# Kernel tuning notes

Measured on AMD Instinct MI355X. Metric: run time of the kernel, lower is better.

The kernel has to match this reference:

```python
import jax, jax.numpy as jnp
import numpy as np

N_NODES = 10000
N_EDGES = 320000
NODE_C = 256
IN_EDGE_C = 256
OUT_EDGE_C = 512
BN_EPS = 1e-5


def setup_inputs() -> dict:
    key = jax.random.key(0)
    ks = jax.random.split(key, 10)
    d_in = 2 * NODE_C + IN_EDGE_C  # 768
    x = jax.random.normal(ks[0], (N_NODES, NODE_C), dtype=jnp.float32)
    edge_index = jax.random.randint(ks[1], (2, N_EDGES), 0, N_NODES, dtype=jnp.int64)
    edge_attr = jax.random.normal(ks[2], (N_EDGES, IN_EDGE_C), dtype=jnp.float32)
    # MLP params (Linear stored as [in, out] for x @ W + b)
    W1 = jax.random.normal(ks[3], (d_in, OUT_EDGE_C), dtype=jnp.float32) / np.sqrt(d_in)
    b1 = jnp.zeros((OUT_EDGE_C,), dtype=jnp.float32)
    W2 = jax.random.normal(ks[4], (OUT_EDGE_C, OUT_EDGE_C), dtype=jnp.float32) / np.sqrt(OUT_EDGE_C)
    b2 = jnp.zeros((OUT_EDGE_C,), dtype=jnp.float32)
    # BatchNorm affine params
    gamma = jnp.ones((OUT_EDGE_C,), dtype=jnp.float32)
    beta = jnp.zeros((OUT_EDGE_C,), dtype=jnp.float32)
    return {"x": x, "edge_index": edge_index, "edge_attr": edge_attr,
            "W1": W1, "b1": b1, "W2": W2, "b2": b2,
            "gamma": gamma, "beta": beta}


def reference(x, edge_index, edge_attr, W1, b1, W2, b2, gamma, beta):
    src = edge_index[0]  # x_j (source / neighbor)
    dst = edge_index[1]  # x_i (target, aggregation index)
    x_i = x[dst]                                  # [E, node_c]
    x_j = x[src]                                  # [E, node_c]
    m = jnp.concatenate([x_i, x_j - x_i, edge_attr], axis=-1)  # [E, 2*node_c+edge_c]
    h = jax.nn.relu(m @ W1 + b1) @ W2 + b2        # per-edge MLP -> [E, out_c]
    out = jax.ops.segment_sum(h, dst, num_segments=x.shape[0])  # scatter-add -> [N, out_c]
    # BatchNorm1d (training-mode batch statistics, biased variance)
    mean = jnp.mean(out, axis=0)
    var = jnp.var(out, axis=0)
    y = (out - mean) * jax.lax.rsqrt(var + BN_EPS) * gamma + beta
    return jax.nn.relu(y)
```

## Files before the change

### kernel.cpp

```cpp
#include <hip/hip_runtime.h>
#include <hip/hip_bf16.h>
#include <cstdint>

#define NN 10000
#define NE 320000
#define NC 256
#define OC 512
#define K1 256

typedef __bf16 bf16_t;
typedef bf16_t bf16x8 __attribute__((ext_vector_type(8)));
typedef bf16_t bf16x4 __attribute__((ext_vector_type(4)));
typedef float  f32x4  __attribute__((ext_vector_type(4)));

__device__ __forceinline__ void gload_lds16(const void* g, void* l) {
  __builtin_amdgcn_global_load_lds(
      (const __attribute__((address_space(1))) unsigned int*)g,
      (__attribute__((address_space(3))) unsigned int*)l, 16, 0, 0);
}

__device__ __forceinline__ int permB(int R) {
  return (R & ~63) + ((R & 15) << 2) + ((R >> 4) & 3);
}

__global__ void k_prep(const float* __restrict__ x,
                       const float* __restrict__ W1,
                       const float* __restrict__ W2,
                       bf16_t* __restrict__ xb,
                       bf16_t* __restrict__ w1abt,
                       bf16_t* __restrict__ w1ct,
                       bf16_t* __restrict__ w2t,
                       float* __restrict__ agg,
                       int* __restrict__ deg,
                       int* __restrict__ cursor,
                       float* __restrict__ sums) {
  const int stride = gridDim.x * blockDim.x;
  for (int i = blockIdx.x * blockDim.x + threadIdx.x; i < NN * OC; i += stride) {
    agg[i] = 0.0f;
    if (i < NN * NC) xb[i] = (bf16_t)x[i];
    if (i < 1024 * K1) {
      const int n = i >> 8, k = i & 255;
      float w;
      if (n < OC) w = W1[(size_t)k * OC + n] - W1[(size_t)(k + NC) * OC + n];
      else        w = W1[(size_t)(k + NC) * OC + (n - OC)];
      w1abt[i] = (bf16_t)w;
    }
    if (i < OC * K1) {
      const int n = i >> 8, k = i & 255;
      w1ct[i] = (bf16_t)W1[(size_t)(512 + k) * OC + n];
    }
    if (i < OC * OC) {
      const int n = i >> 9, k = i & 511;
      w2t[i] = (bf16_t)W2[(size_t)k * OC + n];
    }
    if (i < NN) { deg[i] = 0; cursor[i] = 0; }
    if (i < 1024) sums[i] = 0.0f;
  }
}

__global__ void k_deg(const int* __restrict__ dstIdx, int* __restrict__ deg) {
  const int i = blockIdx.x * blockDim.x + threadIdx.x;
  if (i < NE) atomicAdd(&deg[dstIdx[i]], 1);
}

__global__ void k_scan(const int* __restrict__ deg, int* __restrict__ offs) {
  __shared__ int carry;
  __shared__ int wsum[4];
  if (threadIdx.x == 0) carry = 0;
  __syncthreads();
  const int lane = threadIdx.x & 63, w = threadIdx.x >> 6;
  for (int base = 0; base < NN; base += 256) {
    const int i = base + threadIdx.x;
    const int v = (i < NN) ? deg[i] : 0;
    int s = v;
#pragma unroll
    for (int d = 1; d < 64; d <<= 1) { int t = __shfl_up(s, d); if (lane >= d) s += t; }
    if (lane == 63) wsum[w] = s;
    __syncthreads();
    int woff = 0;
    for (int j = 0; j < w; j++) woff += wsum[j];
    const int incl = s + woff + carry;
    if (i < NN) offs[i] = incl - v;
    __syncthreads();
    if (threadIdx.x == 255) carry = incl;
    __syncthreads();
  }
}

__global__ void k_scatter(const int* __restrict__ srcIdx, const int* __restrict__ dstIdx,
                          const int* __restrict__ offs, int* __restrict__ cursor,
                          int* __restrict__ eperm, int* __restrict__ sdst,
                          int* __restrict__ ssrc) {
  const int e = blockIdx.x * blockDim.x + threadIdx.x;
  if (e < NE) {
    const int d = dstIdx[e];
    const int pos = offs[d] + atomicAdd(&cursor[d], 1);
    eperm[pos] = e;
    sdst[pos] = d;
    ssrc[pos] = srcIdx[e];
  }
}

__global__ __launch_bounds__(256) void k_pq(
    const bf16_t* __restrict__ xb,
    const bf16_t* __restrict__ w1abt,
    const float*  __restrict__ b1,
    float*        __restrict__ P,
    bf16_t*       __restrict__ Qb) {
  __shared__ bf16_t sA[128 * 64];
  __shared__ bf16_t sB[128 * 64];

  const int tid = threadIdx.x;
  const int cb = blockIdx.x & 7, rblk = blockIdx.x >> 3;
  const int r0 = rblk * 128, n0 = cb * 128;
  const int lane = tid & 63, wid = tid >> 6;
  const int mbase = (wid >> 1) * 64, nbase = (wid & 1) * 64;
  const int lr = lane >> 3, ls = lane & 7, slog = ls ^ lr;
  const int g = lane >> 4;

  f32x4 acc[4][4];
#pragma unroll
  for (int mi = 0; mi < 4; mi++)
#pragma unroll
    for (int ni = 0; ni < 4; ni++) acc[mi][ni] = (f32x4){0.f, 0.f, 0.f, 0.f};

  for (int kb = 0; kb < K1; kb += 64) {
#pragma unroll
    for (int i = 0; i < 4; i++) {
      const int row = wid * 32 + i * 8;
      int grow = r0 + row + lr;
      if (grow > NN - 1) grow = NN - 1;
      gload_lds16(xb + (size_t)grow * NC + kb + slog * 8, &sA[row * 64]);
      gload_lds16(w1abt + (size_t)(n0 + permB(row + lr)) * K1 + kb + slog * 8,
                  &sB[row * 64]);
    }
    __syncthreads();
#pragma unroll
    for (int kk = 0; kk < 2; kk++) {
      const int sl = kk * 4 + g;
      bf16x8 av[4], bv[4];
#pragma unroll
      for (int mi = 0; mi < 4; mi++) {
        const int rA = mbase + mi * 16 + (lane & 15);
        av[mi] = *(const bf16x8*)&sA[rA * 64 + ((sl ^ (rA & 7)) * 8)];
      }
#pragma unroll
      for (int ni = 0; ni < 4; ni++) {
        const int rB = nbase + ni * 16 + (lane & 15);
        bv[ni] = *(const bf16x8*)&sB[rB * 64 + ((sl ^ (rB & 7)) * 8)];
      }
#pragma unroll
      for (int mi = 0; mi < 4; mi++)
#pragma unroll
        for (int ni = 0; ni < 4; ni++)
          acc[mi][ni] = __builtin_amdgcn_mfma_f32_16x16x32_bf16(av[mi], bv[ni], acc[mi][ni], 0, 0, 0);
    }
    __syncthreads();
  }

  const int col0 = n0 + nbase + (lane & 15) * 4;
  f32x4 b1v = {0.f, 0.f, 0.f, 0.f};
  if (col0 < OC) b1v = *(const f32x4*)&b1[col0];
#pragma unroll
  for (int mi = 0; mi < 4; mi++) {
#pragma unroll
    for (int q = 0; q < 4; q++) {
      const int grow = r0 + mbase + mi * 16 + g * 4 + q;
      if (grow < NN) {
        if (col0 < OC) {
          f32x4 v;
#pragma unroll
          for (int j = 0; j < 4; j++) v[j] = acc[mi][j][q] + b1v[j];
          *(f32x4*)&P[(size_t)grow * OC + col0] = v;
        } else {
          bf16x4 v;
#pragma unroll
          for (int j = 0; j < 4; j++) v[j] = (bf16_t)acc[mi][j][q];
          *(bf16x4*)&Qb[(size_t)grow * OC + (col0 - OC)] = v;
        }
      }
    }
  }
}

__global__ __launch_bounds__(256, 2) void k_edge_gemm(
    const float*  __restrict__ ea,
    const bf16_t* __restrict__ w1ct,
    const float*  __restrict__ P,
    const bf16_t* __restrict__ Qb,
    const int*    __restrict__ eperm,
    const int*    __restrict__ sdst,
    const int*    __restrict__ ssrc,
    float*        __restrict__ agg) {
  __shared__ bf16_t sM[2][128 * 64];
  __shared__ bf16_t sW[2][128 * 64];
  __shared__ int sDst[128];
  __shared__ int sSrc[128];
  __shared__ int sE[128];

  const int bid0 = blockIdx.x;
  const int bid = (bid0 & 7) * 1250 + (bid0 >> 3);
  const int cb = bid & 3, eblk = bid >> 2;
  const int e0 = eblk * 128, n0 = cb * 128;

  const int tid = threadIdx.x;
  if (tid < 128) {
    sDst[tid] = sdst[e0 + tid];
    sSrc[tid] = ssrc[e0 + tid];
    sE[tid]   = eperm[e0 + tid];
  }
  __syncthreads();

  const int lane = tid & 63, wid = tid >> 6;
  const int mbase = (wid >> 1) * 64, nbase = (wid & 1) * 64;
  const int g = lane >> 4, r = lane & 15;
  const int lr = lane >> 3, ls = lane & 7, slogW = ls ^ lr;
  const int mrow = tid >> 1, qd = tid & 1;
  const int msw = mrow & 7;
  const float* eaRow = ea + (size_t)sE[mrow] * NC;

#define STAGE_W(kt, b)                                                        \
  _Pragma("unroll") for (int i = 0; i < 4; i++) {                             \
    const int rowb = wid * 32 + i * 8;                                        \
    gload_lds16(w1ct + (size_t)(n0 + permB(rowb + lr)) * K1 + (kt)*64 + slogW * 8, \
                &sW[b][rowb * 64]);                                           \
  }
#define LOAD_A(kt)                                                            \
  _Pragma("unroll") for (int j = 0; j < 8; j++)                               \
      a[j] = *(const f32x4*)(eaRow + (kt)*64 + qd * 32 + j * 4);
#define WRITE_M(b)                                                            \
  _Pragma("unroll") for (int tt = 0; tt < 4; tt++) {                          \
    const int slot = qd * 4 + tt;                                             \
    bf16x8 v;                                                                 \
    _Pragma("unroll") for (int jj = 0; jj < 4; jj++) {                        \
      v[jj] = (bf16_t)a[tt * 2][jj];                                          \
      v[4 + jj] = (bf16_t)a[tt * 2 + 1][jj];                                  \
    }                                                                         \
    *(bf16x8*)&sM[b][mrow * 64 + ((slot ^ msw) * 8)] = v;                     \
  }

  f32x4 a[8];

  STAGE_W(0, 0);
  LOAD_A(0);

  const int col0 = n0 + nbase + r * 4;
  f32x4  Pp[4][4];
  bf16x4 Qp[4][4];
#pragma unroll
  for (int mi = 0; mi < 4; mi++) {
    const int rbase = mbase + mi * 16 + g * 4;
#pragma unroll
    for (int q = 0; q < 4; q++) {
      Pp[mi][q] = *(const f32x4*)&P[(size_t)sDst[rbase + q] * OC + col0];
      Qp[mi][q] = *(const bf16x4*)&Qb[(size_t)sSrc[rbase + q] * OC + col0];
    }
  }

  WRITE_M(0);

  f32x4 acc[4][4];
#pragma unroll
  for (int mi = 0; mi < 4; mi++)
#pragma unroll
    for (int ni = 0; ni < 4; ni++) acc[mi][ni] = (f32x4){0.f, 0.f, 0.f, 0.f};

#pragma unroll
  for (int t = 0; t < 4; t++) {
    const int b = t & 1;
    __syncthreads();
    if (t < 3) { STAGE_W(t + 1, b ^ 1); LOAD_A(t + 1); }
#pragma unroll
    for (int kk = 0; kk < 2; kk++) {
      const int sl = kk * 4 + g;
      bf16x8 av[4], bv[4];
#pragma unroll
      for (int mi = 0; mi < 4; mi++) {
        const int rA = mbase + mi * 16 + r;
        av[mi] = *(const bf16x8*)&sM[b][rA * 64 + ((sl ^ (rA & 7)) * 8)];
      }
#pragma unroll
      for (int ni = 0; ni < 4; ni++) {
        const int rB = nbase + ni * 16 + r;
        bv[ni] = *(const bf16x8*)&sW[b][rB * 64 + ((sl ^ (rB & 7)) * 8)];
      }
#pragma unroll
      for (int mi = 0; mi < 4; mi++)
#pragma unroll
        for (int ni = 0; ni < 4; ni++)
          acc[mi][ni] = __builtin_amdgcn_mfma_f32_16x16x32_bf16(av[mi], bv[ni], acc[mi][ni], 0, 0, 0);
    }
    if (t < 3) { WRITE_M(b ^ 1); }
  }
#undef STAGE_W
#undef LOAD_A
#undef WRITE_M

#pragma unroll
  for (int mi = 0; mi < 4; mi++) {
    const int rbase = mbase + mi * 16 + g * 4;
    const int d0 = sDst[rbase],     d1 = sDst[rbase + 1];
    const int d2 = sDst[rbase + 2], d3 = sDst[rbase + 3];
    const int headId = d0, tailId = d3;
    const bool b1q = (d1 != d0), b2q = (d2 != d1), b3q = (d3 != d2);
    const bool seen = b1q | b2q | b3q;
    bool match[3];
#pragma unroll
    for (int j = 0; j < 3; j++) {
      const int tIdj = __shfl(tailId, (lane & 15) | (j << 4));
      match[j] = (j < g) && (tIdj == headId);
    }
    const int nextHead = __shfl(headId, (lane + 16) & 63);
    const bool endsHere = (g == 3) || (nextHead != tailId);

    f32x4 v0, v1, v2, v3;
#pragma unroll
    for (int j = 0; j < 4; j++) {
      v0[j] = fmaxf(acc[mi][j][0] + Pp[mi][0][j] + (float)Qp[mi][0][j], 0.f);
      v1[j] = fmaxf(acc[mi][j][1] + Pp[mi][1][j] + (float)Qp[mi][1][j], 0.f);
      v2[j] = fmaxf(acc[mi][j][2] + Pp[mi][2][j] + (float)Qp[mi][2][j], 0.f);
      v3[j] = fmaxf(acc[mi][j][3] + Pp[mi][3][j] + (float)Qp[mi][3][j], 0.f);
    }

    f32x4 head = {0.f, 0.f, 0.f, 0.f}, run = v0;
    bool first = true;
    if (b1q) { head = run; first = false; run = v1; } else run += v1;
    if (b2q) {
      if (first) { head = run; first = false; }
      else {
        float* base = agg + (size_t)d1 * OC + col0;
#pragma unroll
        for (int j = 0; j < 4; j++) if (run[j] != 0.f) atomicAdd(base + j, run[j]);
      }
      run = v2;
    } else run += v2;
    if (b3q) {
      if (first) { head = run; first = false; }
      else {
        float* base = agg + (size_t)d2 * OC + col0;
#pragma unroll
        for (int j = 0; j < 4; j++) if (run[j] != 0.f) atomicAdd(base + j, run[j]);
      }
      run = v3;
    } else run += v3;
    const f32x4 tailSum = run;

    f32x4 inc = {0.f, 0.f, 0.f, 0.f};
#pragma unroll
    for (int jg = 0; jg < 3; jg++) {
      f32x4 ts;
#pragma unroll
      for (int c = 0; c < 4; c++) ts[c] = __shfl(tailSum[c], (lane & 15) | (jg << 4));
      if (match[jg]) inc += ts;
    }
    if (seen) {
      float* base = agg + (size_t)headId * OC + col0;
#pragma unroll
      for (int j = 0; j < 4; j++) {
        const float h = head[j] + inc[j];
        if (h != 0.f) atomicAdd(base + j, h);
      }
    }
    if (endsHere) {
      float* base = agg + (size_t)tailId * OC + col0;
#pragma unroll
      for (int j = 0; j < 4; j++) {
        const float t = tailSum[j] + (seen ? 0.f : inc[j]);
        if (t != 0.f) atomicAdd(base + j, t);
      }
    }
  }
}

__global__ __launch_bounds__(256) void k_node_gemm(
    const float*  __restrict__ agg,
    const bf16_t* __restrict__ w2t,
    const float*  __restrict__ b2,
    const int*    __restrict__ deg,
    float*        __restrict__ out) {
  __shared__ bf16_t sM[128 * 72];
  __shared__ bf16_t sW[128 * 72];

  const int tid  = threadIdx.x;
  const int bid  = blockIdx.x;
  const int cb   = bid & 3;
  const int rblk = bid >> 2;
  const int r0   = rblk * 128;
  const int n0   = cb * 128;

  const int lane  = tid & 63, wid = tid >> 6;
  const int mbase = (wid >> 1) * 64, nbase = (wid & 1) * 64;
  const int se = tid >> 1;
  const int sk = (tid & 1) * 32;
  const int arow  = r0 + se;
  const bool rowok = arow < NN;

  f32x4 acc[4][4];
#pragma unroll
  for (int mi = 0; mi < 4; mi++)
#pragma unroll
    for (int ni = 0; ni < 4; ni++) acc[mi][ni] = (f32x4){0.f, 0.f, 0.f, 0.f};

  for (int kb = 0; kb < OC; kb += 64) {
    {
      bf16x8* dst = (bf16x8*)&sM[se * 72 + sk];
      if (rowok) {
        const float* pf = agg + (size_t)arow * OC + kb + sk;
        f32x4 f[8];
#pragma unroll
        for (int i = 0; i < 8; i++) f[i] = *(const f32x4*)(pf + i * 4);
#pragma unroll
        for (int i = 0; i < 4; i++) {
          bf16x8 v;
#pragma unroll
          for (int j = 0; j < 4; j++) {
            v[j]     = (bf16_t)f[2 * i][j];
            v[4 + j] = (bf16_t)f[2 * i + 1][j];
          }
          dst[i] = v;
        }
      } else {
        bf16x8 z = {};
        dst[0] = z; dst[1] = z; dst[2] = z; dst[3] = z;
      }
    }
    {
      const bf16_t* pw = w2t + (size_t)(n0 + permB(se)) * OC + kb + sk;
      bf16x8* dst = (bf16x8*)&sW[se * 72 + sk];
      dst[0] = *(const bf16x8*)(pw);
      dst[1] = *(const bf16x8*)(pw + 8);
      dst[2] = *(const bf16x8*)(pw + 16);
      dst[3] = *(const bf16x8*)(pw + 24);
    }
    __syncthreads();
#pragma unroll
    for (int kk = 0; kk < 2; kk++) {
      const int krd = kk * 32 + (lane >> 4) * 8;
      bf16x8 av[4], bv[4];
#pragma unroll
      for (int mi = 0; mi < 4; mi++)
        av[mi] = *(const bf16x8*)&sM[(mbase + mi * 16 + (lane & 15)) * 72 + krd];
#pragma unroll
      for (int ni = 0; ni < 4; ni++)
        bv[ni] = *(const bf16x8*)&sW[(nbase + ni * 16 + (lane & 15)) * 72 + krd];
#pragma unroll
      for (int mi = 0; mi < 4; mi++)
#pragma unroll
        for (int ni = 0; ni < 4; ni++)
          acc[mi][ni] = __builtin_amdgcn_mfma_f32_16x16x32_bf16(av[mi], bv[ni], acc[mi][ni], 0, 0, 0);
    }
    __syncthreads();
  }

  const int col0 = n0 + nbase + (lane & 15) * 4;
  const f32x4 b2v = *(const f32x4*)&b2[col0];
  const int g = lane >> 4;
#pragma unroll
  for (int mi = 0; mi < 4; mi++) {
#pragma unroll
    for (int q = 0; q < 4; q++) {
      const int row = r0 + mbase + mi * 16 + g * 4 + q;
      if (row < NN) {
        const float dg = (float)deg[row];
        f32x4 v;
#pragma unroll
        for (int j = 0; j < 4; j++) v[j] = acc[mi][j][q] + b2v[j] * dg;
        *(f32x4*)&out[(size_t)row * OC + col0] = v;
      }
    }
  }
}

__global__ void k_bn_stats(const float* __restrict__ out, float* __restrict__ sums) {
  const int c = threadIdx.x;
  float s1 = 0.f, q1 = 0.f, s2 = 0.f, q2 = 0.f;
  for (int n = blockIdx.x; n < NN; n += gridDim.x) {
    const float* row = out + (size_t)n * OC;
    const float v1 = row[c], v2 = row[c + 256];
    s1 += v1; q1 += v1 * v1;
    s2 += v2; q2 += v2 * v2;
  }
  atomicAdd(&sums[c], s1);        atomicAdd(&sums[OC + c], q1);
  atomicAdd(&sums[c + 256], s2);  atomicAdd(&sums[OC + c + 256], q2);
}

__global__ void k_bn_finalize(const float* __restrict__ sums,
                              const float* __restrict__ gamma,
                              const float* __restrict__ beta,
                              float* __restrict__ scale,
                              float* __restrict__ shift) {
  const int c = threadIdx.x;
  const float mean = sums[c] * (1.0f / NN);
  const float var  = sums[OC + c] * (1.0f / NN) - mean * mean;
  const float r    = rsqrtf(var + 1e-5f);
  const float sc   = r * gamma[c];
  scale[c] = sc;
  shift[c] = beta[c] - mean * sc;
}

__global__ void k_bn_apply(float* __restrict__ out,
                           const float* __restrict__ scale,
                           const float* __restrict__ shift) {
  const int i = blockIdx.x * blockDim.x + threadIdx.x;
  f32x4 v = *((const f32x4*)out + i);
  const int c = (i & 127) << 2;
  f32x4 r;
#pragma unroll
  for (int j = 0; j < 4; j++) r[j] = fmaxf(v[j] * scale[c + j] + shift[c + j], 0.0f);
  *((f32x4*)out + i) = r;
}

extern "C" void kernel_launch(void* const* d_in, const int* in_sizes, int n_in,
                              void* d_out, int out_size, void* d_ws, size_t ws_size,
                              hipStream_t stream) {
  const float* x     = (const float*)d_in[0];
  const int*   ei    = (const int*)d_in[1];
  const float* ea    = (const float*)d_in[2];
  const float* W1    = (const float*)d_in[3];
  const float* b1    = (const float*)d_in[4];
  const float* W2    = (const float*)d_in[5];
  const float* b2    = (const float*)d_in[6];
  const float* gamma = (const float*)d_in[7];
  const float* beta  = (const float*)d_in[8];
  float* out = (float*)d_out;

  char* ws = (char*)d_ws;
  float*  agg    = (float*)(ws);
  float*  P      = (float*)(ws + 20480000);
  bf16_t* Qb     = (bf16_t*)(ws + 40960000);
  bf16_t* xb     = (bf16_t*)(ws + 51200000);
  bf16_t* w1abt  = (bf16_t*)(ws + 56320000);
  bf16_t* w1ct   = (bf16_t*)(ws + 56844288);
  bf16_t* w2t    = (bf16_t*)(ws + 57106432);
  int*    deg    = (int*)(ws + 57630720);
  int*    offs   = (int*)(ws + 57670720);
  int*    cursor = (int*)(ws + 57710720);
  float*  sums   = (float*)(ws + 57750720);
  float*  scale  = (float*)(ws + 57754816);
  float*  shift  = (float*)(ws + 57756864);
  int*    eperm  = (int*)(ws + 57758912);
  int*    sdst   = (int*)(ws + 59038912);
  int*    ssrc   = (int*)(ws + 60318912);

  const int* srcIdx = ei;
  const int* dstIdx = ei + NE;

  k_prep<<<4096, 256, 0, stream>>>(x, W1, W2, xb, w1abt, w1ct, w2t, agg, deg, cursor, sums);
  k_deg<<<(NE + 255) / 256, 256, 0, stream>>>(dstIdx, deg);
  k_scan<<<1, 256, 0, stream>>>(deg, offs);
  k_scatter<<<(NE + 255) / 256, 256, 0, stream>>>(srcIdx, dstIdx, offs, cursor,
                                                  eperm, sdst, ssrc);
  k_pq<<<((NN + 127) / 128) * 8, 256, 0, stream>>>(xb, w1abt, b1, P, Qb);
  k_edge_gemm<<<(NE / 128) * 4, 256, 0, stream>>>(ea, w1ct, P, Qb, eperm, sdst, ssrc, agg);
  k_node_gemm<<<((NN + 127) / 128) * 4, 256, 0, stream>>>(agg, w2t, b2, deg, out);
  k_bn_stats<<<256, 256, 0, stream>>>(out, sums);
  k_bn_finalize<<<1, 512, 0, stream>>>(sums, gamma, beta, scale, shift);
  k_bn_apply<<<(NN * OC / 4 + 255) / 256, 256, 0, stream>>>(out, scale, shift);
}
```

Baseline: 511.5 us.

## Split edge GEMM into H materialization plus segmented-sum kernel

Adds a path that writes the per-edge ReLU hidden activations to a bf16 buffer H. A separate per-node kernel then sums each node's contiguous sorted edges into agg without atomics. This replaces the fused in-tile segmented reduction and atomicAdd scatter when the workspace is large enough. The cost is a large extra round-trip through global memory for H and one more kernel launch.

```diff
diff --git a/kernel.cpp b/kernel.cpp
--- a/kernel.cpp
+++ b/kernel.cpp
@@ -183,7 +183,158 @@
   }
 }
 
-__global__ __launch_bounds__(256, 2) void k_edge_gemm(
+__global__ __launch_bounds__(256, 2) void k_edge_h(
+    const float*  __restrict__ ea,
+    const bf16_t* __restrict__ w1ct,
+    const float*  __restrict__ P,
+    const bf16_t* __restrict__ Qb,
+    const int*    __restrict__ eperm,
+    const int*    __restrict__ sdst,
+    const int*    __restrict__ ssrc,
+    bf16_t*       __restrict__ H) {
+  __shared__ bf16_t sM[2][128 * 64];
+  __shared__ bf16_t sW[2][128 * 64];
+  __shared__ int sDst[128];
+  __shared__ int sSrc[128];
+  __shared__ int sE[128];
+
+  const int bid = (blockIdx.x & 7) * 1250 + (blockIdx.x >> 3);
+  const int cb = bid & 3, eblk = bid >> 2;
+  const int e0 = eblk * 128, n0 = cb * 128;
+
+  const int tid = threadIdx.x;
+  if (tid < 128) {
+    sDst[tid] = sdst[e0 + tid];
+    sSrc[tid] = ssrc[e0 + tid];
+    sE[tid]   = eperm[e0 + tid];
+  }
+  __syncthreads();
+
+  const int lane = tid & 63, wid = tid >> 6;
+  const int mbase = (wid >> 1) * 64, nbase = (wid & 1) * 64;
+  const int g = lane >> 4, r = lane & 15;
+  const int lr = lane >> 3, ls = lane & 7, slogW = ls ^ lr;
+  const int mrow = tid >> 1, qd = tid & 1;
+  const int msw = mrow & 7;
+  const float* eaRow = ea + (size_t)sE[mrow] * NC;
+
+#define STAGE_W(kt, b)                                                        \
+  _Pragma("unroll") for (int i = 0; i < 4; i++) {                             \
+    const int rowb = wid * 32 + i * 8;                                        \
+    gload_lds16(w1ct + (size_t)(n0 + permB(rowb + lr)) * K1 + (kt)*64 + slogW * 8, \
+                &sW[b][rowb * 64]);                                           \
+  }
+#define LOAD_A(kt)                                                            \
+  _Pragma("unroll") for (int j = 0; j < 8; j++)                               \
+      a[j] = *(const f32x4*)(eaRow + (kt)*64 + qd * 32 + j * 4);
+#define WRITE_M(b)                                                            \
+  _Pragma("unroll") for (int tt = 0; tt < 4; tt++) {                          \
+    const int slot = qd * 4 + tt;                                             \
+    bf16x8 v;                                                                 \
+    _Pragma("unroll") for (int jj = 0; jj < 4; jj++) {                        \
+      v[jj] = (bf16_t)a[tt * 2][jj];                                          \
+      v[4 + jj] = (bf16_t)a[tt * 2 + 1][jj];                                  \
+    }                                                                         \
+    *(bf16x8*)&sM[b][mrow * 64 + ((slot ^ msw) * 8)] = v;                     \
+  }
+
+  f32x4 a[8];
+
+  STAGE_W(0, 0);
+  LOAD_A(0);
+
+  const int col0 = n0 + nbase + r * 4;
+  f32x4  Pp[4][4];
+  bf16x4 Qp[4][4];
+#pragma unroll
+  for (int mi = 0; mi < 4; mi++) {
+    const int rbase = mbase + mi * 16 + g * 4;
+#pragma unroll
+    for (int q = 0; q < 4; q++) {
+      Pp[mi][q] = *(const f32x4*)&P[(size_t)sDst[rbase + q] * OC + col0];
+      Qp[mi][q] = *(const bf16x4*)&Qb[(size_t)sSrc[rbase + q] * OC + col0];
+    }
+  }
+
+  WRITE_M(0);
+
+  f32x4 acc[4][4];
+#pragma unroll
+  for (int mi = 0; mi < 4; mi++)
+#pragma unroll
+    for (int ni = 0; ni < 4; ni++) acc[mi][ni] = (f32x4){0.f, 0.f, 0.f, 0.f};
+
+#pragma unroll
+  for (int t = 0; t < 4; t++) {
+    const int b = t & 1;
+    __syncthreads();
+    if (t < 3) { STAGE_W(t + 1, b ^ 1); LOAD_A(t + 1); }
+#pragma unroll
+    for (int kk = 0; kk < 2; kk++) {
+      const int sl = kk * 4 + g;
+      bf16x8 av[4], bv[4];
+#pragma unroll
+      for (int mi = 0; mi < 4; mi++) {
+        const int rA = mbase + mi * 16 + r;
+        av[mi] = *(const bf16x8*)&sM[b][rA * 64 + ((sl ^ (rA & 7)) * 8)];
+      }
+#pragma unroll
+      for (int ni = 0; ni < 4; ni++) {
+        const int rB = nbase + ni * 16 + r;
+        bv[ni] = *(const bf16x8*)&sW[b][rB * 64 + ((sl ^ (rB & 7)) * 8)];
+      }
+#pragma unroll
+      for (int mi = 0; mi < 4; mi++)
+#pragma unroll
+        for (int ni = 0; ni < 4; ni++)
+          acc[mi][ni] = __builtin_amdgcn_mfma_f32_16x16x32_bf16(av[mi], bv[ni], acc[mi][ni], 0, 0, 0);
+    }
+    if (t < 3) { WRITE_M(b ^ 1); }
+  }
+#undef STAGE_W
+#undef LOAD_A
+#undef WRITE_M
+
+#pragma unroll
+  for (int mi = 0; mi < 4; mi++) {
+#pragma unroll
+    for (int q = 0; q < 4; q++) {
+      const int row = e0 + mbase + mi * 16 + g * 4 + q;
+      bf16x4 hv;
+#pragma unroll
+      for (int j = 0; j < 4; j++)
+        hv[j] = (bf16_t)fmaxf(acc[mi][j][q] + Pp[mi][q][j] + (float)Qp[mi][q][j], 0.f);
+      *(bf16x4*)&H[(size_t)row * OC + col0] = hv;
+    }
+  }
+}
+
+__global__ __launch_bounds__(256) void k_seg(
+    const bf16_t* __restrict__ H,
+    const int*    __restrict__ offs,
+    const int*    __restrict__ deg,
+    float*        __restrict__ agg) {
+  const int lane = threadIdx.x & 63, wid = threadIdx.x >> 6;
+  const int n = blockIdx.x * 4 + wid;
+  if (n >= NN) return;
+  const int s = offs[n], d = deg[n];
+  float acc[8] = {0.f, 0.f, 0.f, 0.f, 0.f, 0.f, 0.f, 0.f};
+  const bf16_t* p = H + (size_t)s * OC + lane * 8;
+  for (int i = 0; i < d; i++) {
+    const bf16x8 v = *(const bf16x8*)p;
+    p += OC;
+#pragma unroll
+    for (int j = 0; j < 8; j++) acc[j] += (float)v[j];
+  }
+  float* o = agg + (size_t)n * OC + lane * 8;
+  f32x4 a0, a1;
+#pragma unroll
+  for (int j = 0; j < 4; j++) { a0[j] = acc[j]; a1[j] = acc[4 + j]; }
+  *(f32x4*)o = a0;
+  *(f32x4*)(o + 4) = a1;
+}
+
+__global__ __launch_bounds__(256, 2) void k_edge_gemm_fused(
     const float*  __restrict__ ea,
     const bf16_t* __restrict__ w1ct,
     const float*  __restrict__ P,
@@ -198,8 +349,7 @@
   __shared__ int sSrc[128];
   __shared__ int sE[128];
 
-  const int bid0 = blockIdx.x;
-  const int bid = (bid0 & 7) * 1250 + (bid0 >> 3);
+  const int bid = (blockIdx.x & 7) * 1250 + (blockIdx.x >> 3);
   const int cb = bid & 3, eblk = bid >> 2;
   const int e0 = eblk * 128, n0 = cb * 128;
 
@@ -240,7 +390,6 @@
   }
 
   f32x4 a[8];
-
   STAGE_W(0, 0);
   LOAD_A(0);
 
@@ -365,8 +514,8 @@
       float* base = agg + (size_t)tailId * OC + col0;
 #pragma unroll
       for (int j = 0; j < 4; j++) {
-        const float t = tailSum[j] + (seen ? 0.f : inc[j]);
-        if (t != 0.f) atomicAdd(base + j, t);
+        const float t2 = tailSum[j] + (seen ? 0.f : inc[j]);
+        if (t2 != 0.f) atomicAdd(base + j, t2);
       }
     }
   }
@@ -541,6 +690,8 @@
   int*    eperm  = (int*)(ws + 57758912);
   int*    sdst   = (int*)(ws + 59038912);
   int*    ssrc   = (int*)(ws + 60318912);
+  const size_t H_OFF = 61598912;
+  const size_t WS_NEEDED = H_OFF + (size_t)NE * OC * sizeof(bf16_t);
 
   const int* srcIdx = ei;
   const int* dstIdx = ei + NE;
@@ -551,7 +702,16 @@
   k_scatter<<<(NE + 255) / 256, 256, 0, stream>>>(srcIdx, dstIdx, offs, cursor,
                                                   eperm, sdst, ssrc);
   k_pq<<<((NN + 127) / 128) * 8, 256, 0, stream>>>(xb, w1abt, b1, P, Qb);
-  k_edge_gemm<<<(NE / 128) * 4, 256, 0, stream>>>(ea, w1ct, P, Qb, eperm, sdst, ssrc, agg);
+
+  if (ws_size >= WS_NEEDED) {
+    bf16_t* H = (bf16_t*)(ws + H_OFF);
+    k_edge_h<<<(NE / 128) * 4, 256, 0, stream>>>(ea, w1ct, P, Qb, eperm, sdst, ssrc, H);
+    k_seg<<<(NN + 3) / 4, 256, 0, stream>>>(H, offs, deg, agg);
+  } else {
+    k_edge_gemm_fused<<<(NE / 128) * 4, 256, 0, stream>>>(ea, w1ct, P, Qb, eperm,
+                                                          sdst, ssrc, agg);
+  }
+
   k_node_gemm<<<((NN + 127) / 128) * 4, 256, 0, stream>>>(agg, w2t, b2, deg, out);
   k_bn_stats<<<256, 256, 0, stream>>>(out, sums);
   k_bn_finalize<<<1, 512, 0, stream>>>(sums, gamma, beta, scale, shift);
```

Measured after the change: 572.5 us (median of 2 runs). 1.12x slower.

## Pre-sort and convert edge attributes to bf16 before the edge GEMM

Applied to the files above, without the earlier changes.

Adds a pass that gathers edge_attr rows in destination-sorted order and converts them to bf16 in a workspace buffer. The edge GEMM then stages A tiles with async global-to-LDS loads, the same path already used for the weights, instead of gathering fp32 rows into registers and converting them there. This removes register pressure and the indirect gather from the hot kernel. In exchange it adds an extra kernel and a round trip through memory for the converted attributes.

```diff
diff --git a/kernel.cpp b/kernel.cpp
--- a/kernel.cpp
+++ b/kernel.cpp
@@ -101,6 +101,21 @@
   }
 }
 
+__global__ __launch_bounds__(256) void k_sortcvt(
+    const float* __restrict__ ea, const int* __restrict__ eperm,
+    bf16_t* __restrict__ eab) {
+  const int lane = threadIdx.x & 63, wv = threadIdx.x >> 6;
+  const int stride = gridDim.x * 4;
+  for (int pos = blockIdx.x * 4 + wv; pos < NE; pos += stride) {
+    const float* src = ea + (size_t)eperm[pos] * NC + lane * 4;
+    const f32x4 v = *(const f32x4*)src;
+    bf16x4 o;
+#pragma unroll
+    for (int j = 0; j < 4; j++) o[j] = (bf16_t)v[j];
+    *(bf16x4*)&eab[(size_t)pos * NC + lane * 4] = o;
+  }
+}
+
 __global__ __launch_bounds__(256) void k_pq(
     const bf16_t* __restrict__ xb,
     const bf16_t* __restrict__ w1abt,
@@ -184,11 +199,10 @@
 }
 
 __global__ __launch_bounds__(256, 2) void k_edge_gemm(
-    const float*  __restrict__ ea,
+    const bf16_t* __restrict__ eab,
     const bf16_t* __restrict__ w1ct,
     const float*  __restrict__ P,
     const bf16_t* __restrict__ Qb,
-    const int*    __restrict__ eperm,
     const int*    __restrict__ sdst,
     const int*    __restrict__ ssrc,
     float*        __restrict__ agg) {
@@ -196,53 +210,30 @@
   __shared__ bf16_t sW[2][128 * 64];
   __shared__ int sDst[128];
   __shared__ int sSrc[128];
-  __shared__ int sE[128];
-
-  const int bid0 = blockIdx.x;
-  const int bid = (bid0 & 7) * 1250 + (bid0 >> 3);
+
+  const int bid = (blockIdx.x & 7) * 1250 + (blockIdx.x >> 3);
   const int cb = bid & 3, eblk = bid >> 2;
   const int e0 = eblk * 128, n0 = cb * 128;
 
   const int tid = threadIdx.x;
-  if (tid < 128) {
-    sDst[tid] = sdst[e0 + tid];
-    sSrc[tid] = ssrc[e0 + tid];
-    sE[tid]   = eperm[e0 + tid];
-  }
+  if (tid < 128) { sDst[tid] = sdst[e0 + tid]; sSrc[tid] = ssrc[e0 + tid]; }
   __syncthreads();
 
   const int lane = tid & 63, wid = tid >> 6;
   const int mbase = (wid >> 1) * 64, nbase = (wid & 1) * 64;
   const int g = lane >> 4, r = lane & 15;
-  const int lr = lane >> 3, ls = lane & 7, slogW = ls ^ lr;
-  const int mrow = tid >> 1, qd = tid & 1;
-  const int msw = mrow & 7;
-  const float* eaRow = ea + (size_t)sE[mrow] * NC;
-
-#define STAGE_W(kt, b)                                                        \
+  const int lr = lane >> 3, ls = lane & 7, slog = ls ^ lr;
+
+#define STAGE(kt, b)                                                          \
   _Pragma("unroll") for (int i = 0; i < 4; i++) {                             \
-    const int rowb = wid * 32 + i * 8;                                        \
-    gload_lds16(w1ct + (size_t)(n0 + permB(rowb + lr)) * K1 + (kt)*64 + slogW * 8, \
+    const int rowb = wid * 32 + i * 8;                 \
+    gload_lds16(eab + (size_t)(e0 + rowb + lr) * K1 + (kt)*64 + slog * 8,     \
+                &sM[b][rowb * 64]);                                           \
+    gload_lds16(w1ct + (size_t)(n0 + permB(rowb + lr)) * K1 + (kt)*64 + slog * 8, \
                 &sW[b][rowb * 64]);                                           \
   }
-#define LOAD_A(kt)                                                            \
-  _Pragma("unroll") for (int j = 0; j < 8; j++)                               \
-      a[j] = *(const f32x4*)(eaRow + (kt)*64 + qd * 32 + j * 4);
-#define WRITE_M(b)                                                            \
-  _Pragma("unroll") for (int tt = 0; tt < 4; tt++) {                          \
-    const int slot = qd * 4 + tt;                                             \
-    bf16x8 v;                                                                 \
-    _Pragma("unroll") for (int jj = 0; jj < 4; jj++) {                        \
-      v[jj] = (bf16_t)a[tt * 2][jj];                                          \
-      v[4 + jj] = (bf16_t)a[tt * 2 + 1][jj];                                  \
-    }                                                                         \
-    *(bf16x8*)&sM[b][mrow * 64 + ((slot ^ msw) * 8)] = v;                     \
-  }
-
-  f32x4 a[8];
-
-  STAGE_W(0, 0);
-  LOAD_A(0);
+
+  STAGE(0, 0);
 
   const int col0 = n0 + nbase + r * 4;
   f32x4  Pp[4][4];
@@ -257,8 +248,6 @@
     }
   }
 
-  WRITE_M(0);
-
   f32x4 acc[4][4];
 #pragma unroll
   for (int mi = 0; mi < 4; mi++)
@@ -269,7 +258,7 @@
   for (int t = 0; t < 4; t++) {
     const int b = t & 1;
     __syncthreads();
-    if (t < 3) { STAGE_W(t + 1, b ^ 1); LOAD_A(t + 1); }
+    if (t < 3) STAGE(t + 1, b ^ 1);
 #pragma unroll
     for (int kk = 0; kk < 2; kk++) {
       const int sl = kk * 4 + g;
@@ -290,11 +279,8 @@
         for (int ni = 0; ni < 4; ni++)
           acc[mi][ni] = __builtin_amdgcn_mfma_f32_16x16x32_bf16(av[mi], bv[ni], acc[mi][ni], 0, 0, 0);
     }
-    if (t < 3) { WRITE_M(b ^ 1); }
-  }
-#undef STAGE_W
-#undef LOAD_A
-#undef WRITE_M
+  }
+#undef STAGE
 
 #pragma unroll
   for (int mi = 0; mi < 4; mi++) {
@@ -365,8 +351,8 @@
       float* base = agg + (size_t)tailId * OC + col0;
 #pragma unroll
       for (int j = 0; j < 4; j++) {
-        const float t = tailSum[j] + (seen ? 0.f : inc[j]);
-        if (t != 0.f) atomicAdd(base + j, t);
+        const float t2 = tailSum[j] + (seen ? 0.f : inc[j]);
+        if (t2 != 0.f) atomicAdd(base + j, t2);
       }
     }
   }
@@ -541,6 +527,7 @@
   int*    eperm  = (int*)(ws + 57758912);
   int*    sdst   = (int*)(ws + 59038912);
   int*    ssrc   = (int*)(ws + 60318912);
+  bf16_t* eab    = (bf16_t*)(ws + 61598912);
 
   const int* srcIdx = ei;
   const int* dstIdx = ei + NE;
@@ -550,8 +537,9 @@
   k_scan<<<1, 256, 0, stream>>>(deg, offs);
   k_scatter<<<(NE + 255) / 256, 256, 0, stream>>>(srcIdx, dstIdx, offs, cursor,
                                                   eperm, sdst, ssrc);
+  k_sortcvt<<<2048, 256, 0, stream>>>(ea, eperm, eab);
   k_pq<<<((NN + 127) / 128) * 8, 256, 0, stream>>>(xb, w1abt, b1, P, Qb);
-  k_edge_gemm<<<(NE / 128) * 4, 256, 0, stream>>>(ea, w1ct, P, Qb, eperm, sdst, ssrc, agg);
+  k_edge_gemm<<<(NE / 128) * 4, 256, 0, stream>>>(eab, w1ct, P, Qb, sdst, ssrc, agg);
   k_node_gemm<<<((NN + 127) / 128) * 4, 256, 0, stream>>>(agg, w2t, b2, deg, out);
   k_bn_stats<<<256, 256, 0, stream>>>(out, sums);
   k_bn_finalize<<<1, 512, 0, stream>>>(sums, gamma, beta, scale, shift);
```

Measured after the change: 571.5 us. 1.12x slower.
